# Kernel optimization log

Hardware: AMD Instinct MI355X
Metric: run time of the kernel (lower is better)

## Reference

```python
import jax, jax.numpy as jnp
import numpy as np

INV_SQRT2 = 0.7071067811865476


def _quadrature_ops(d):
    # truncated harmonic-oscillator ladder operator: a[n, n+1] = sqrt(n+1)
    a = jnp.diag(jnp.sqrt(jnp.arange(1, d, dtype=jnp.float32)), k=1)
    X0 = (a + a.T) * INV_SQRT2
    P0 = (a - a.T) * INV_SQRT2  # real-valued stand-in for the momentum quadrature
    I = jnp.eye(d, dtype=jnp.float32)
    return I, X0, P0


def setup_inputs() -> dict:
    key = jax.random.key(0)
    ks = jax.random.split(key, 6)
    D, d, w, K = 512, 32, 8, 4
    return {
        "mps_params": jax.random.normal(ks[0], (D, d, D), dtype=jnp.float32),
        "theta": jax.random.normal(ks[1], (1,), dtype=jnp.float32),
        "env_L": jax.random.normal(ks[2], (K, D, w, D), dtype=jnp.float32) * 0.1,
        "env_R": jax.random.normal(ks[3], (K, D, w, D), dtype=jnp.float32) * 0.1,
        "coeffs": jax.random.normal(ks[4], (K, w, w, 5), dtype=jnp.float32),
        "prefactors": jax.random.normal(ks[5], (K,), dtype=jnp.float32),
    }


def reference(mps_params, theta, env_L, env_R, coeffs, prefactors):
    A = mps_params  # [D(left), d(phys), D(right)]
    d = A.shape[1]
    K = prefactors.shape[0]

    # norm_fn: psi.H @ psi for a single-tensor MPS is sum(A^2)
    An = A / jnp.sqrt(jnp.sum(A * A))

    # _get_XandP: quadrature rotation from basis params
    I, X0, P0 = _quadrature_ops(d)
    c, s = jnp.cos(theta[0]), jnp.sin(theta[0])
    X = c * X0 + s * P0
    P = -s * X0 + c * P0

    # dynamic MPO cores: W_k[i,j] = sum_c coeffs[k,i,j,c] * ops[c]
    ops = jnp.stack([I, X, P, X @ X, P @ P])  # [5, d, d]
    W = jnp.einsum('kijc,cab->kijab', coeffs, ops)  # [K, w, w, d, d]

    out = jnp.zeros((), dtype=A.dtype)
    for k in range(K):  # fixed small loop over Hamiltonian constituents
        # T: [L, w, p, r]
        T = jnp.einsum('Lwl,lpr->Lwpr', env_L[k], An)
        # apply MPO core: [L, v, P, r]
        T = jnp.einsum('wvPp,Lwpr->LvPr', W[k], T)
        # close with right env: [L, P, R]
        T = jnp.einsum('LvPr,Rvr->LPR', T, env_R[k])
        out = out + prefactors[k] * jnp.einsum('LPR,LPR->', An, T)
    return out
```

## Files before the change

### kernel.cpp

```cpp
#include <hip/hip_runtime.h>


typedef __attribute__((ext_vector_type(8))) _Float16 f16x8;
typedef __attribute__((ext_vector_type(4))) float f32x4;

__device__ __forceinline__ unsigned short f2h(float f) {
    _Float16 h = (_Float16)f;
    return *(unsigned short*)&h;
}

__device__ __forceinline__ void gload16(const void* g, void* l) {
    __builtin_amdgcn_global_load_lds(
        (const __attribute__((address_space(1))) void*)g,
        (__attribute__((address_space(3))) void*)l, 16, 0, 0);
}

struct GArg {
    const unsigned short* A;
    const unsigned short* B;
    unsigned short* C;
    int kshift;
    long long kextra;
};

__device__ __forceinline__ void stage32(
    const GArg& g, int srow0, int col0, int kt0,
    short* dstA, short* dstB, int tid)
{
    #pragma unroll
    for (int q = 0; q < 2; ++q) {
        const int c = q * 512 + tid;
        const int row = c >> 2;
        const int gs = (c & 3) ^ (row & 3);
        const int gr = srow0 + row;
        const size_t aoff = (size_t)gr * 512 + (size_t)((unsigned)gr >> g.kshift) * g.kextra;
        gload16(g.A + aoff + kt0 + gs * 8, dstA + c * 8);
    }
    {
        const int c = tid;
        const int row = c >> 2;
        const int gs = (c & 3) ^ (row & 3);
        gload16(g.B + (size_t)(col0 + row) * 512 + kt0 + gs * 8, dstB + c * 8);
    }
}

__global__ __launch_bounds__(512, 4) void gemm_dual_mega(int NPB, GArg g0, GArg g1)
{
    __shared__ short lds[28928];
    const GArg g = blockIdx.z ? g1 : g0;
    const int tid = threadIdx.x;
    const int wid = tid >> 6, lane = tid & 63;
    const int wm = wid >> 1, wn = wid & 1;
    const int lrow = lane & 15, lgrp = lane >> 4;
    const int rdoff = lrow * 32 + ((lgrp ^ (lrow & 3)) * 8);

    const int xcd = blockIdx.x & 7, loc = blockIdx.x >> 3;
    const int col0 = (xcd * 16 + loc) * 128;
    const int row_base = blockIdx.y * NPB * 256;

    short* A0 = lds;
    short* A1 = lds + 8192;
    short* B0 = lds + 16384;
    short* B1 = lds + 20480;
    short* repk = lds + 24576;

    const int NT = NPB * 16;

    f32x4 acc[4][4] = {};

    stage32(g, row_base, col0, 0, A0, B0, tid);
    stage32(g, row_base, col0, 32, A1, B1, tid);
    asm volatile("s_waitcnt vmcnt(3)" ::: "memory");
    __builtin_amdgcn_s_barrier();
    __builtin_amdgcn_sched_barrier(0);

    for (int it = 0; it < NT; ++it) {
        const short* cA = (it & 1) ? A1 : A0;
        const short* cB = (it & 1) ? B1 : B0;
        short* wA = (it & 1) ? A1 : A0;
        short* wB = (it & 1) ? B1 : B0;

        f16x8 afr[4], bfr[4];
        #pragma unroll
        for (int j = 0; j < 4; ++j)
            bfr[j] = *(const f16x8*)&cB[(wn * 64 + j * 16) * 32 + rdoff];
        #pragma unroll
        for (int i = 0; i < 4; ++i)
            afr[i] = *(const f16x8*)&cA[(wm * 64 + i * 16) * 32 + rdoff];
        asm volatile("s_waitcnt lgkmcnt(0)" ::: "memory");
        __builtin_amdgcn_sched_barrier(0);
        __builtin_amdgcn_s_barrier();
        __builtin_amdgcn_sched_barrier(0);
        if (it + 2 < NT) {
            const int it2 = it + 2;
            stage32(g, row_base + (it2 >> 4) * 256, col0, (it2 & 15) * 32, wA, wB, tid);
        }
        __builtin_amdgcn_s_setprio(1);
        #pragma unroll
        for (int i = 0; i < 4; ++i)
            #pragma unroll
            for (int j = 0; j < 4; ++j)
                acc[i][j] = __builtin_amdgcn_mfma_f32_16x16x32_f16(afr[i], bfr[j], acc[i][j], 0, 0, 0);
        __builtin_amdgcn_s_setprio(0);
        __builtin_amdgcn_sched_barrier(0);
        if (it + 2 < NT) asm volatile("s_waitcnt vmcnt(3)" ::: "memory");
        else             asm volatile("s_waitcnt vmcnt(0)" ::: "memory");
        __builtin_amdgcn_sched_barrier(0);
        __builtin_amdgcn_s_barrier();
        __builtin_amdgcn_sched_barrier(0);

        if ((it & 15) == 15) {
            const int row0 = row_base + (it >> 4) * 256;
            const int orow = lgrp * 4, ocol = lrow;
            #pragma unroll
            for (int c8 = 0; c8 < 8; ++c8) {
                if (wm == (c8 >> 1)) {
                    const int ib = (c8 & 1) * 2;
                    #pragma unroll
                    for (int di = 0; di < 2; ++di)
                        #pragma unroll
                        for (int j = 0; j < 4; ++j)
                            #pragma unroll
                            for (int q = 0; q < 4; ++q)
                                repk[(di * 16 + orow + q) * 136 + wn * 64 + j * 16 + ocol] =
                                    (short)f2h(acc[ib + di][j][q]);
                }
                asm volatile("s_waitcnt lgkmcnt(0)" ::: "memory");
                __builtin_amdgcn_s_barrier();
                {
                    const int rr = tid >> 4, cc = tid & 15;
                    *(int4*)(g.C + (size_t)(row0 + c8 * 32 + rr) * 16384 + col0 + cc * 8) =
                        *(const int4*)&repk[rr * 136 + cc * 8];
                }
                asm volatile("s_waitcnt lgkmcnt(0)" ::: "memory");
                __builtin_amdgcn_s_barrier();
            }
            #pragma unroll
            for (int i = 0; i < 4; ++i)
                #pragma unroll
                for (int j = 0; j < 4; ++j)
                    acc[i][j] = (f32x4){0.f, 0.f, 0.f, 0.f};
        }
    }
}

__global__ __launch_bounds__(1024) void gemm_g4w(
    const unsigned short* __restrict__ T1, const unsigned short* __restrict__ Yp,
    const float* __restrict__ W2p, float* __restrict__ dacc,
    int Lt8, int zkShift, int BKC)
{
    __shared__ short sh[16384];
    const int tid = threadIdx.x;
    const int wid = tid >> 6, lane = tid & 63;
    const int kidx = blockIdx.x >> zkShift;
    const int kz = (blockIdx.x - (kidx << zkShift)) * BKC;
    const int wr = (wid >> 2) * 64, wc = (wid & 3) * 64;
    const int lrow = lane & 15, kb = (lane >> 4) * 8;

    const int r = tid >> 2, kc = (tid & 3) * 8;
    const int w_ = r >> 5, p_ = r & 31;
    const size_t T1k = (size_t)kidx * Lt8 * 16384;
    const size_t Yk = (size_t)kidx * 4096;
    const size_t aoff = T1k + (size_t)w_ * 16384 + (size_t)p_ * 512;
    const size_t boff = Yk + (size_t)p_ * 16384 + (size_t)w_ * 512;

    f32x4 acc[4][4] = {};

    for (int k0 = 0; k0 < BKC; k0 += 32) {
        const int kk = kz + k0;
        const int lt = kk >> 9, rbase = kk & 511;
        gload16(T1 + aoff + (size_t)lt * 131072 + rbase + kc, sh + tid * 8);
        gload16(Yp + boff + (size_t)lt * 524288 + rbase + kc, sh + 8192 + tid * 8);
        __syncthreads();
        f16x8 a[4], b[4];
        #pragma unroll
        for (int i = 0; i < 4; ++i)
            a[i] = *(const f16x8*)&sh[(wr + i * 16 + lrow) * 32 + kb];
        #pragma unroll
        for (int j = 0; j < 4; ++j)
            b[j] = *(const f16x8*)&sh[8192 + (wc + j * 16 + lrow) * 32 + kb];
        #pragma unroll
        for (int i = 0; i < 4; ++i)
            #pragma unroll
            for (int j = 0; j < 4; ++j)
                acc[i][j] = __builtin_amdgcn_mfma_f32_16x16x32_f16(a[i], b[j], acc[i][j], 0, 0, 0);
        __syncthreads();
    }

    const int orow = (lane >> 4) * 4, ocol = lane & 15;
    const float* Wk = W2p + ((size_t)kidx << 16);
    float s = 0.f;
    #pragma unroll
    for (int j = 0; j < 4; ++j) {
        const int n = wc + j * 16 + ocol;
        const float* wrow = Wk + (size_t)n * 256 + wr + orow;
        #pragma unroll
        for (int i = 0; i < 4; ++i) {
            float4 wv = *(const float4*)(wrow + i * 16);
            s += wv.x * acc[i][j][0] + wv.y * acc[i][j][1]
               + wv.z * acc[i][j][2] + wv.w * acc[i][j][3];
        }
    }
    __syncthreads();
    float* red = (float*)sh;
    red[tid] = s;
    __syncthreads();
    for (int st = 512; st > 0; st >>= 1) {
        if (tid < st) red[tid] += red[tid + st];
        __syncthreads();
    }
    if (tid == 0) atomicAdd(dacc, red[0]);
}

__global__ __launch_bounds__(256) void cast_sumsq(
    const float* __restrict__ in, unsigned short* __restrict__ out,
    long long n4, float* __restrict__ sumsq)
{
    float p = 0.f;
    for (long long i = (long long)blockIdx.x * blockDim.x + threadIdx.x; i < n4;
         i += (long long)gridDim.x * blockDim.x) {
        float4 v = ((const float4*)in)[i];
        p += v.x * v.x + v.y * v.y + v.z * v.z + v.w * v.w;
        union { unsigned short s[4]; uint2 d; } o;
        o.s[0] = f2h(v.x); o.s[1] = f2h(v.y); o.s[2] = f2h(v.z); o.s[3] = f2h(v.w);
        ((uint2*)out)[i] = o.d;
    }
    __shared__ float sh[256];
    sh[threadIdx.x] = p;
    __syncthreads();
    for (int s = 128; s > 0; s >>= 1) {
        if (threadIdx.x < s) sh[threadIdx.x] += sh[threadIdx.x + s];
        __syncthreads();
    }
    if (threadIdx.x == 0) atomicAdd(sumsq, sh[0]);
}

__global__ void cast_kernel(const float* __restrict__ in, unsigned short* __restrict__ out,
                            long long n4)
{
    for (long long i = (long long)blockIdx.x * blockDim.x + threadIdx.x; i < n4;
         i += (long long)gridDim.x * blockDim.x) {
        float4 v = ((const float4*)in)[i];
        union { unsigned short s[4]; uint2 d; } o;
        o.s[0] = f2h(v.x); o.s[1] = f2h(v.y); o.s[2] = f2h(v.z); o.s[3] = f2h(v.w);
        ((uint2*)out)[i] = o.d;
    }
}

__global__ void transpose_cast(const float* __restrict__ in, unsigned short* __restrict__ out,
                               int R, int C, long long in_stride, long long out_stride)
{
    __shared__ float tile[32][33];
    in += (long long)blockIdx.z * in_stride;
    out += (long long)blockIdx.z * out_stride;
    int c0 = blockIdx.x * 32, r0 = blockIdx.y * 32;
    int tx = threadIdx.x, ty = threadIdx.y;
    #pragma unroll
    for (int i = 0; i < 4; ++i)
        tile[ty + i * 8][tx] = in[(size_t)(r0 + ty + i * 8) * C + c0 + tx];
    __syncthreads();
    #pragma unroll
    for (int i = 0; i < 4; ++i)
        out[(size_t)(c0 + ty + i * 8) * R + r0 + tx] = f2h(tile[tx][ty + i * 8]);
}

__global__ void build_ops(const float* __restrict__ theta, float* __restrict__ ops)
{
    __shared__ float X[32][32], Pm[32][32];
    int i = threadIdx.y, j = threadIdx.x;
    float c = cosf(theta[0]), s = sinf(theta[0]);
    float aij = (j == i + 1) ? sqrtf((float)j) : 0.f;
    float aji = (i == j + 1) ? sqrtf((float)i) : 0.f;
    const float inv = 0.70710678118654752440f;
    float x0 = (aij + aji) * inv;
    float p0 = (aij - aji) * inv;
    X[i][j] = c * x0 + s * p0;
    Pm[i][j] = -s * x0 + c * p0;
    __syncthreads();
    float xx = 0.f, pp = 0.f;
    #pragma unroll
    for (int m = 0; m < 32; ++m) {
        xx += X[i][m] * X[m][j];
        pp += Pm[i][m] * Pm[m][j];
    }
    ops[0 * 1024 + i * 32 + j] = (i == j) ? 1.f : 0.f;
    ops[1 * 1024 + i * 32 + j] = X[i][j];
    ops[2 * 1024 + i * 32 + j] = Pm[i][j];
    ops[3 * 1024 + i * 32 + j] = xx;
    ops[4 * 1024 + i * 32 + j] = pp;
}

__global__ void build_w(const float* __restrict__ coeffs, const float* __restrict__ ops,
                        const float* __restrict__ pref, float* __restrict__ W2)
{
    int b = blockIdx.x;
    int k = b >> 6, w = (b >> 3) & 7, v = b & 7;
    int P = threadIdx.y, p = threadIdx.x;
    const float* cf = coeffs + ((k * 8 + w) * 8 + v) * 5;
    float acc = 0.f;
    #pragma unroll
    for (int c = 0; c < 5; ++c) acc += cf[c] * ops[c * 1024 + P * 32 + p];
    W2[(size_t)k * 65536 + (v * 32 + P) * 256 + (w * 32 + p)] = acc * pref[k];
}

__global__ void finalize_kernel(const float* __restrict__ dacc, const float* __restrict__ sumsq,
                                float* __restrict__ out)
{
    if (threadIdx.x == 0) out[0] = dacc[0] / sumsq[0];
}

extern "C" void kernel_launch(void* const* d_in, const int* in_sizes, int n_in,
                              void* d_out, int out_size, void* d_ws, size_t ws_size,
                              hipStream_t stream)
{
    const float* A      = (const float*)d_in[0];
    const float* theta  = (const float*)d_in[1];
    const float* envL   = (const float*)d_in[2];
    const float* envR   = (const float*)d_in[3];
    const float* coeffs = (const float*)d_in[4];
    const float* pref   = (const float*)d_in[5];
    float* out = (float*)d_out;

    char* ws = (char*)d_ws;
    float* sumsq = (float*)ws;
    float* dacc  = (float*)(ws + 4);
    float* ops   = (float*)(ws + 64);
    float* W2    = (float*)(ws + (32 << 10));
    unsigned short* envLh  = (unsigned short*)(ws + (4ull << 20));
    unsigned short* Ah     = (unsigned short*)(ws + (21ull << 20));
    unsigned short* Ath    = (unsigned short*)(ws + (38ull << 20));
    unsigned short* envRth = (unsigned short*)(ws + (55ull << 20));
    const size_t big0 = 72ull << 20;

    int Lt = 512;
    while (Lt > 16) {
        size_t need = big0 + 2ull * (size_t)Lt * (1ull << 20);
        if (need <= ws_size) break;
        Lt >>= 1;
    }
    unsigned short* T1 = (unsigned short*)(ws + big0);
    unsigned short* Yp = T1 + (size_t)Lt * 524288;

    const int Lt8 = Lt * 8;
    const int kshiftA = __builtin_ctz(Lt8);
    const long long kextraA = 2097152LL - (long long)Lt8 * 512;
    const int NPB = Lt / 16;
    const int KT = Lt * 512;
    int BKC = KT / 64; if (BKC < 128) BKC = 128;
    const int zk = KT / BKC;
    const int zkShift = __builtin_ctz(zk);

    hipMemsetAsync(ws, 0, 64, stream);

    cast_sumsq<<<1024, 256, 0, stream>>>(A, Ah, 2097152LL, sumsq);
    build_ops<<<1, dim3(32, 32), 0, stream>>>(theta, ops);
    build_w<<<256, dim3(32, 32), 0, stream>>>(coeffs, ops, pref, W2);
    cast_kernel<<<2048, 256, 0, stream>>>(envL, envLh, 2097152LL);
    transpose_cast<<<dim3(512, 16, 1), dim3(32, 8), 0, stream>>>(A, Ath, 512, 16384, 0, 0);
    transpose_cast<<<dim3(128, 16, 4), dim3(32, 8), 0, stream>>>(envR, envRth, 512, 4096,
                                                                 2097152LL, 2097152LL);

    const int ntiles = 512 / Lt;
    for (int t = 0; t < ntiles; ++t) {
        GArg g0, g1;
        g0.A = envLh + (size_t)t * Lt8 * 512; g0.B = Ath; g0.C = T1;
        g0.kshift = kshiftA; g0.kextra = kextraA;
        g1.A = Ah + (size_t)t * Lt * 16384; g1.B = envRth; g1.C = Yp;
        g1.kshift = 30; g1.kextra = 0;
        gemm_dual_mega<<<dim3(128, 2, 2), 512, 0, stream>>>(NPB, g0, g1);
        gemm_g4w<<<dim3(4 * zk), 1024, 0, stream>>>(T1, Yp, W2, dacc, Lt8, zkShift, BKC);
    }
    finalize_kernel<<<1, 64, 0, stream>>>(dacc, sumsq, out);
}
```

Measured before the change: 1.098 ms.

## Restructure dual GEMM and contraction kernels into smaller chunked tiles with more waves

```diff
diff --git a/kernel.cpp b/kernel.cpp
--- a/kernel.cpp
+++ b/kernel.cpp
@@ -28,49 +28,49 @@
     short* dstA, short* dstB, int tid)
 {
     #pragma unroll
-    for (int q = 0; q < 2; ++q) {
-        const int c = q * 512 + tid;
+    for (int q = 0; q < 4; ++q) {
+        const int c = q * 256 + tid;
         const int row = c >> 2;
-        const int gs = (c & 3) ^ (row & 3);
+        const int gs = (c & 3) ^ ((row >> 1) & 3);
         const int gr = srow0 + row;
         const size_t aoff = (size_t)gr * 512 + (size_t)((unsigned)gr >> g.kshift) * g.kextra;
         gload16(g.A + aoff + kt0 + gs * 8, dstA + c * 8);
     }
-    {
-        const int c = tid;
+    #pragma unroll
+    for (int q = 0; q < 2; ++q) {
+        const int c = q * 256 + tid;
         const int row = c >> 2;
-        const int gs = (c & 3) ^ (row & 3);
+        const int gs = (c & 3) ^ ((row >> 1) & 3);
         gload16(g.B + (size_t)(col0 + row) * 512 + kt0 + gs * 8, dstB + c * 8);
     }
 }
 
-__global__ __launch_bounds__(512, 4) void gemm_dual_mega(int NPB, GArg g0, GArg g1)
-{
-    __shared__ short lds[28928];
+__global__ __launch_bounds__(256, 2) void gemm_dual(int K, GArg g0, GArg g1)
+{
+    __shared__ short lds[24576];
     const GArg g = blockIdx.z ? g1 : g0;
     const int tid = threadIdx.x;
     const int wid = tid >> 6, lane = tid & 63;
     const int wm = wid >> 1, wn = wid & 1;
     const int lrow = lane & 15, lgrp = lane >> 4;
-    const int rdoff = lrow * 32 + ((lgrp ^ (lrow & 3)) * 8);
+    const int rdoff = lrow * 32 + ((lgrp ^ ((lrow >> 1) & 3)) * 8);
 
     const int xcd = blockIdx.x & 7, loc = blockIdx.x >> 3;
     const int col0 = (xcd * 16 + loc) * 128;
-    const int row_base = blockIdx.y * NPB * 256;
+    const int row0 = blockIdx.y * 256;
 
     short* A0 = lds;
     short* A1 = lds + 8192;
     short* B0 = lds + 16384;
     short* B1 = lds + 20480;
-    short* repk = lds + 24576;
-
-    const int NT = NPB * 16;
-
-    f32x4 acc[4][4] = {};
-
-    stage32(g, row_base, col0, 0, A0, B0, tid);
-    stage32(g, row_base, col0, 32, A1, B1, tid);
-    asm volatile("s_waitcnt vmcnt(3)" ::: "memory");
+
+    const int NT = K >> 5;
+
+    f32x4 acc[8][4] = {};
+
+    stage32(g, row0, col0, 0, A0, B0, tid);
+    stage32(g, row0, col0, 32, A1, B1, tid);
+    asm volatile("s_waitcnt vmcnt(6)" ::: "memory");
     __builtin_amdgcn_s_barrier();
     __builtin_amdgcn_sched_barrier(0);
 
@@ -80,71 +80,64 @@
         short* wA = (it & 1) ? A1 : A0;
         short* wB = (it & 1) ? B1 : B0;
 
-        f16x8 afr[4], bfr[4];
+        f16x8 afr[8], bfr[4];
         #pragma unroll
         for (int j = 0; j < 4; ++j)
             bfr[j] = *(const f16x8*)&cB[(wn * 64 + j * 16) * 32 + rdoff];
         #pragma unroll
-        for (int i = 0; i < 4; ++i)
-            afr[i] = *(const f16x8*)&cA[(wm * 64 + i * 16) * 32 + rdoff];
+        for (int i = 0; i < 8; ++i)
+            afr[i] = *(const f16x8*)&cA[(wm * 128 + i * 16) * 32 + rdoff];
         asm volatile("s_waitcnt lgkmcnt(0)" ::: "memory");
         __builtin_amdgcn_sched_barrier(0);
         __builtin_amdgcn_s_barrier();
         __builtin_amdgcn_sched_barrier(0);
-        if (it + 2 < NT) {
-            const int it2 = it + 2;
-            stage32(g, row_base + (it2 >> 4) * 256, col0, (it2 & 15) * 32, wA, wB, tid);
-        }
+        if (it + 2 < NT)
+            stage32(g, row0, col0, (it + 2) * 32, wA, wB, tid);
         __builtin_amdgcn_s_setprio(1);
         #pragma unroll
-        for (int i = 0; i < 4; ++i)
+        for (int i = 0; i < 8; ++i)
             #pragma unroll
             for (int j = 0; j < 4; ++j)
                 acc[i][j] = __builtin_amdgcn_mfma_f32_16x16x32_f16(afr[i], bfr[j], acc[i][j], 0, 0, 0);
         __builtin_amdgcn_s_setprio(0);
         __builtin_amdgcn_sched_barrier(0);
-        if (it + 2 < NT) asm volatile("s_waitcnt vmcnt(3)" ::: "memory");
+        if (it + 2 < NT) asm volatile("s_waitcnt vmcnt(6)" ::: "memory");
         else             asm volatile("s_waitcnt vmcnt(0)" ::: "memory");
         __builtin_amdgcn_sched_barrier(0);
         __builtin_amdgcn_s_barrier();
         __builtin_amdgcn_sched_barrier(0);
-
-        if ((it & 15) == 15) {
-            const int row0 = row_base + (it >> 4) * 256;
-            const int orow = lgrp * 4, ocol = lrow;
+    }
+
+    short* repk = lds;
+    const int orow = lgrp * 4, ocol = lrow;
+    #pragma unroll
+    for (int c8 = 0; c8 < 8; ++c8) {
+        if (wm == (c8 >> 2)) {
+            const int ib = (c8 & 3) * 2;
             #pragma unroll
-            for (int c8 = 0; c8 < 8; ++c8) {
-                if (wm == (c8 >> 1)) {
-                    const int ib = (c8 & 1) * 2;
-                    #pragma unroll
-                    for (int di = 0; di < 2; ++di)
-                        #pragma unroll
-                        for (int j = 0; j < 4; ++j)
-                            #pragma unroll
-                            for (int q = 0; q < 4; ++q)
-                                repk[(di * 16 + orow + q) * 136 + wn * 64 + j * 16 + ocol] =
-                                    (short)f2h(acc[ib + di][j][q]);
-                }
-                asm volatile("s_waitcnt lgkmcnt(0)" ::: "memory");
-                __builtin_amdgcn_s_barrier();
-                {
-                    const int rr = tid >> 4, cc = tid & 15;
-                    *(int4*)(g.C + (size_t)(row0 + c8 * 32 + rr) * 16384 + col0 + cc * 8) =
-                        *(const int4*)&repk[rr * 136 + cc * 8];
-                }
-                asm volatile("s_waitcnt lgkmcnt(0)" ::: "memory");
-                __builtin_amdgcn_s_barrier();
-            }
-            #pragma unroll
-            for (int i = 0; i < 4; ++i)
+            for (int di = 0; di < 2; ++di)
                 #pragma unroll
                 for (int j = 0; j < 4; ++j)
-                    acc[i][j] = (f32x4){0.f, 0.f, 0.f, 0.f};
+                    #pragma unroll
+                    for (int q = 0; q < 4; ++q)
+                        repk[(di * 16 + orow + q) * 136 + wn * 64 + j * 16 + ocol] =
+                            (short)f2h(acc[ib + di][j][q]);
         }
-    }
-}
-
-__global__ __launch_bounds__(1024) void gemm_g4w(
+        asm volatile("s_waitcnt lgkmcnt(0)" ::: "memory");
+        __builtin_amdgcn_s_barrier();
+        #pragma unroll
+        for (int s2 = 0; s2 < 2; ++s2) {
+            const int idx = s2 * 256 + tid;
+            const int rr = idx >> 4, cc = idx & 15;
+            *(int4*)(g.C + (size_t)(row0 + c8 * 32 + rr) * 16384 + col0 + cc * 8) =
+                *(const int4*)&repk[rr * 136 + cc * 8];
+        }
+        asm volatile("s_waitcnt lgkmcnt(0)" ::: "memory");
+        __builtin_amdgcn_s_barrier();
+    }
+}
+
+__global__ __launch_bounds__(512, 1) void gemm_g4w(
     const unsigned short* __restrict__ T1, const unsigned short* __restrict__ Yp,
     const float* __restrict__ W2p, float* __restrict__ dacc,
     int Lt8, int zkShift, int BKC)
@@ -154,48 +147,54 @@
     const int wid = tid >> 6, lane = tid & 63;
     const int kidx = blockIdx.x >> zkShift;
     const int kz = (blockIdx.x - (kidx << zkShift)) * BKC;
-    const int wr = (wid >> 2) * 64, wc = (wid & 3) * 64;
-    const int lrow = lane & 15, kb = (lane >> 4) * 8;
-
-    const int r = tid >> 2, kc = (tid & 3) * 8;
-    const int w_ = r >> 5, p_ = r & 31;
+    const int wm = wid >> 2, wn = wid & 3;
+    const int lrow = lane & 15, lgrp = lane >> 4;
+    const int rdoff = lrow * 32 + ((lgrp ^ ((lrow >> 1) & 3)) * 8);
+
     const size_t T1k = (size_t)kidx * Lt8 * 16384;
     const size_t Yk = (size_t)kidx * 4096;
-    const size_t aoff = T1k + (size_t)w_ * 16384 + (size_t)p_ * 512;
-    const size_t boff = Yk + (size_t)p_ * 16384 + (size_t)w_ * 512;
-
-    f32x4 acc[4][4] = {};
+
+    f32x4 acc[8][4] = {};
 
     for (int k0 = 0; k0 < BKC; k0 += 32) {
         const int kk = kz + k0;
         const int lt = kk >> 9, rbase = kk & 511;
-        gload16(T1 + aoff + (size_t)lt * 131072 + rbase + kc, sh + tid * 8);
-        gload16(Yp + boff + (size_t)lt * 524288 + rbase + kc, sh + 8192 + tid * 8);
+        #pragma unroll
+        for (int q = 0; q < 2; ++q) {
+            const int c = q * 512 + tid;
+            const int row = c >> 2;
+            const int gs = (c & 3) ^ ((row >> 1) & 3);
+            const int hi = row >> 5, lo = row & 31;
+            gload16(T1 + T1k + (size_t)(lt * 8 + hi) * 16384 + lo * 512 + rbase + gs * 8,
+                    sh + c * 8);
+            gload16(Yp + Yk + (size_t)(lt * 32 + lo) * 16384 + hi * 512 + rbase + gs * 8,
+                    sh + 8192 + c * 8);
+        }
         __syncthreads();
-        f16x8 a[4], b[4];
-        #pragma unroll
-        for (int i = 0; i < 4; ++i)
-            a[i] = *(const f16x8*)&sh[(wr + i * 16 + lrow) * 32 + kb];
+        f16x8 a[8], b[4];
         #pragma unroll
         for (int j = 0; j < 4; ++j)
-            b[j] = *(const f16x8*)&sh[8192 + (wc + j * 16 + lrow) * 32 + kb];
-        #pragma unroll
-        for (int i = 0; i < 4; ++i)
+            b[j] = *(const f16x8*)&sh[8192 + (wn * 64 + j * 16) * 32 + rdoff];
+        #pragma unroll
+        for (int i = 0; i < 8; ++i)
+            a[i] = *(const f16x8*)&sh[(wm * 128 + i * 16) * 32 + rdoff];
+        #pragma unroll
+        for (int i = 0; i < 8; ++i)
             #pragma unroll
             for (int j = 0; j < 4; ++j)
                 acc[i][j] = __builtin_amdgcn_mfma_f32_16x16x32_f16(a[i], b[j], acc[i][j], 0, 0, 0);
         __syncthreads();
     }
 
-    const int orow = (lane >> 4) * 4, ocol = lane & 15;
+    const int orow = lgrp * 4, ocol = lrow;
     const float* Wk = W2p + ((size_t)kidx << 16);
     float s = 0.f;
     #pragma unroll
     for (int j = 0; j < 4; ++j) {
-        const int n = wc + j * 16 + ocol;
-        const float* wrow = Wk + (size_t)n * 256 + wr + orow;
-        #pragma unroll
-        for (int i = 0; i < 4; ++i) {
+        const int n = wn * 64 + j * 16 + ocol;
+        const float* wrow = Wk + (size_t)n * 256 + wm * 128 + orow;
+        #pragma unroll
+        for (int i = 0; i < 8; ++i) {
             float4 wv = *(const float4*)(wrow + i * 16);
             s += wv.x * acc[i][j][0] + wv.y * acc[i][j][1]
                + wv.z * acc[i][j][2] + wv.w * acc[i][j][3];
@@ -205,7 +204,7 @@
     float* red = (float*)sh;
     red[tid] = s;
     __syncthreads();
-    for (int st = 512; st > 0; st >>= 1) {
+    for (int st = 256; st > 0; st >>= 1) {
         if (tid < st) red[tid] += red[tid + st];
         __syncthreads();
     }
@@ -332,7 +331,7 @@
     unsigned short* envRth = (unsigned short*)(ws + (55ull << 20));
     const size_t big0 = 72ull << 20;
 
-    int Lt = 512;
+    int Lt = 64;
     while (Lt > 16) {
         size_t need = big0 + 2ull * (size_t)Lt * (1ull << 20);
         if (need <= ws_size) break;
@@ -344,9 +343,8 @@
     const int Lt8 = Lt * 8;
     const int kshiftA = __builtin_ctz(Lt8);
     const long long kextraA = 2097152LL - (long long)Lt8 * 512;
-    const int NPB = Lt / 16;
     const int KT = Lt * 512;
-    int BKC = KT / 64; if (BKC < 128) BKC = 128;
+    const int BKC = 512;
     const int zk = KT / BKC;
     const int zkShift = __builtin_ctz(zk);
 
@@ -367,8 +365,8 @@
         g0.kshift = kshiftA; g0.kextra = kextraA;
         g1.A = Ah + (size_t)t * Lt * 16384; g1.B = envRth; g1.C = Yp;
         g1.kshift = 30; g1.kextra = 0;
-        gemm_dual_mega<<<dim3(128, 2, 2), 512, 0, stream>>>(NPB, g0, g1);
-        gemm_g4w<<<dim3(4 * zk), 1024, 0, stream>>>(T1, Yp, W2, dacc, Lt8, zkShift, BKC);
+        gemm_dual<<<dim3(128, (Lt * 32) / 256, 2), 256, 0, stream>>>(512, g0, g1);
+        gemm_g4w<<<dim3(4 * zk), 512, 0, stream>>>(T1, Yp, W2, dacc, Lt8, zkShift, BKC);
     }
     finalize_kernel<<<1, 64, 0, stream>>>(dacc, sumsq, out);
 }
```

New measurement: 1.047 ms. 4.7% less time.
